# Performance work log

Measured on AMD Instinct MI355X. Metric: run time of the kernel, lower is better.

## Reference

```python
import jax, jax.numpy as jnp
import numpy as np

HIDDEN_DIM = 64


def setup_inputs() -> dict:
    key = jax.random.key(0)
    k1, k2, k3, k4, k5 = jax.random.split(key, 5)
    B, C, H, W = 4, HIDDEN_DIM, 80, 80
    query = jax.random.normal(k1, (B, C, H, W), dtype=jnp.float32)
    keys = jax.random.normal(k2, (B, C, H, W), dtype=jnp.float32)
    values = jax.random.normal(k3, (B, C, H, W), dtype=jnp.float32)
    # 1x1 conv == per-pixel linear: weight [C_out, C_in], bias [C_out]
    fan_in = C  # kernel_size=1 -> fan_in = C*1*1
    bound = 1.0 / np.sqrt(fan_in)
    Wq = jax.random.uniform(k4, (C, C), dtype=jnp.float32, minval=-bound, maxval=bound)
    bq = jax.random.uniform(k5, (C,), dtype=jnp.float32, minval=-bound, maxval=bound)
    return {"query": query, "keys": keys, "values": values, "Wq": Wq, "bq": bq}


def reference(query, keys, values, Wq, bq):
    B, C, H, W = query.shape
    scale = C ** (-0.5)
    # 1x1 conv projection of query
    qp = jnp.einsum('bchw,dc->bdhw', query, Wq) + bq[None, :, None, None]
    q = qp.reshape(B, C, H * W).transpose(0, 2, 1)       # [B, N, C]
    k = keys.reshape(B, C, H * W)                        # [B, C, N]
    attn = jax.nn.softmax(jnp.einsum('bnc,bcm->bnm', q, k) * scale, axis=-1)  # [B, N, N]
    v = values.reshape(B, C, H * W).transpose(0, 2, 1)   # [B, N, C]
    context = jnp.einsum('bnm,bmc->bnc', attn, v)        # [B, N, C]
    return context.transpose(0, 2, 1).reshape(B, C, H, W)
```

## Files before the change

kernel.cpp:

```cpp
#include <hip/hip_runtime.h>
#include <hip/hip_bf16.h>


#define NPIX 6400
#define SZ 1638400
#define SHIFT2 11.541560327111707f

typedef float f32x4 __attribute__((ext_vector_type(4)));
typedef short bf16x8 __attribute__((ext_vector_type(8)));

#if defined(__has_builtin)
#if __has_builtin(__builtin_amdgcn_sched_barrier)
#define SCHED_FENCE() __builtin_amdgcn_sched_barrier(0)
#endif
#if __has_builtin(__builtin_amdgcn_exp2f)
#define EXP2(x) __builtin_amdgcn_exp2f(x)
#endif
#endif
#ifndef SCHED_FENCE
#define SCHED_FENCE()
#endif
#ifndef EXP2
#define EXP2(x) exp2f(x)
#endif

__device__ __forceinline__ void split2(float x, short& h, short& l) {
  unsigned xb = __float_as_uint(x);
  h = (short)(xb >> 16);
  float r = x - __uint_as_float(xb & 0xffff0000u);
  l = (short)(__float_as_uint(r) >> 16);
}

__device__ __forceinline__ short rne_bf16(float x) {
  unsigned u = __float_as_uint(x);
  return (short)((u + 0x7fffu + ((u >> 16) & 1u)) >> 16);
}

__device__ __forceinline__ unsigned pk2(float a, float b) {
  __hip_bfloat162 t = __float22bfloat162_rn(make_float2(a, b));
  unsigned r;
  __builtin_memcpy(&r, &t, 4);
  return r;
}

__global__ __launch_bounds__(256, 4) void prep(
    const float* __restrict__ query, const float* __restrict__ keys,
    const float* __restrict__ values, const float* __restrict__ Wq,
    const float* __restrict__ bq, short* __restrict__ ws)
{
  const int tid = threadIdx.x;
  const int w = tid >> 6;
  const int lane = tid & 63, l16 = lane & 15, qq = lane >> 4;
  short* Qh = ws;          short* Ql = ws + SZ;
  short* Kh = ws + 2 * SZ; short* Kl = ws + 3 * SZ;
  short* Vh = ws + 4 * SZ;
  const int x = blockIdx.x;

  __shared__ float T[64 * 65];

  if (x < 400) {
    const int b = x / 100, t64 = x % 100;
    const int m0 = t64 * 64;
    const float* kb = keys + (size_t)b * 64 * NPIX;
    {
      const int ch = tid >> 2, ml = (tid & 3) * 4;
      const float* src = kb + (size_t)ch * NPIX + m0 + ml;
      #pragma unroll
      for (int u = 0; u < 4; ++u)
        *(float4*)&T[ch * 65 + ml + 16 * u] = *(const float4*)(src + 16 * u);
    }
    __syncthreads();
    const int mi = t64 * 4 + w;
    #pragma unroll
    for (int c0 = 0; c0 < 2; ++c0) {
      float t[8];
      #pragma unroll
      for (int j = 0; j < 8; ++j)
        t[j] = T[(32 * c0 + 8 * qq + j) * 65 + 16 * w + l16];
      bf16x8 h8, l8;
      #pragma unroll
      for (int j = 0; j < 8; ++j) { short h, l; split2(t[j], h, l); h8[j] = h; l8[j] = l; }
      const int off = ((b * 400 + mi) * 2 + c0) * 512 + lane * 8;
      *(bf16x8*)(Kh + off) = h8;
      *(bf16x8*)(Kl + off) = l8;
    }
  } else if (x < 800) {
    const int y = x - 400;
    const int b = y / 100, t64 = y % 100;
    const int r0 = t64 * 64;
    const float* qb = query + (size_t)b * 64 * NPIX;
    {
      const int ch = tid >> 2, ml = (tid & 3) * 4;
      const float* src = qb + (size_t)ch * NPIX + r0 + ml;
      #pragma unroll
      for (int u = 0; u < 4; ++u)
        *(float4*)&T[ch * 65 + ml + 16 * u] = *(const float4*)(src + 16 * u);
    }
    __syncthreads();

    {
      float xv[64];
      #pragma unroll
      for (int cin = 0; cin < 64; ++cin)
        xv[cin] = T[cin * 65 + lane];
      __syncthreads();

      #pragma unroll 4
      for (int c16 = 0; c16 < 16; ++c16) {
        const int co = __builtin_amdgcn_readfirstlane(16 * w + c16);
        const float* row = Wq + co * 64;
        float a = 0.f;
        #pragma unroll
        for (int cin = 0; cin < 64; ++cin)
          a += row[cin] * xv[cin];
        T[co * 65 + lane] = (a + bq[co]) * 0.18033688011112042f;
      }
    }
    __syncthreads();

    const int mi = t64 * 4 + w;
    #pragma unroll
    for (int c0 = 0; c0 < 2; ++c0) {
      float t[8];
      #pragma unroll
      for (int j = 0; j < 8; ++j)
        t[j] = T[(32 * c0 + 8 * qq + j) * 65 + 16 * w + l16];
      bf16x8 h8, l8;
      #pragma unroll
      for (int j = 0; j < 8; ++j) { short h, l; split2(t[j], h, l); h8[j] = h; l8[j] = l; }
      const int off = ((b * 400 + mi) * 2 + c0) * 512 + lane * 8;
      *(bf16x8*)(Qh + off) = h8;
      *(bf16x8*)(Ql + off) = l8;
    }
  } else {
    const int gw = (x - 800) * 4 + w;
    const int b = gw / 200, rest = gw % 200;
    const int i = rest / 2, half = rest % 2;
    const float* vb = values + (size_t)b * 64 * NPIX;
    #pragma unroll
    for (int cc = 0; cc < 2; ++cc) {
      const int ct = 2 * half + cc;
      #pragma unroll
      for (int mh = 0; mh < 2; ++mh) {
        const float* vp = vb + (size_t)(16 * ct + l16) * NPIX + 64 * i + 32 * mh + 8 * qq;
        const float4 a  = *(const float4*)vp;
        const float4 b4 = *(const float4*)(vp + 4);
        const float t[8] = {a.x, a.y, a.z, a.w, b4.x, b4.y, b4.z, b4.w};
        bf16x8 h8;
        #pragma unroll
        for (int j = 0; j < 8; ++j) h8[j] = rne_bf16(t[j]);
        const int off = (((b * 100 + i) * 8) + ct * 2 + mh) * 512 + lane * 8;
        *(bf16x8*)(Vh + off) = h8;
      }
    }
  }
}

__global__ __launch_bounds__(512, 1) void attn_main(
    const short* __restrict__ ws, float* __restrict__ out)
{
  const int tid  = threadIdx.x;
  const int w    = tid >> 6;
  const int lane = tid & 63;
  const int l16  = lane & 15, qq = lane >> 4;
  const int x = blockIdx.x;
  const int b      = x & 3;
  const int rowjob = x >> 2;
  const int rb     = rowjob * 64;

  const short* Qh = ws;
  const short* Kh = ws + 2 * SZ;
  const short* Vh = ws + 4 * SZ;
  float* ob = out + (size_t)b * 64 * NPIX;

  __shared__ char smem[43008];
  short* P   = ((short*)smem) + (w << 11);
  short* QL  = ((short*)smem) + 16384;
  float* OC  = (float*)smem;
  float* LST = (float*)(smem + 40960);

  bf16x8 qfh[4][2];
  {
    const short* qp = Qh + (size_t)((b * 400 + rowjob * 4) * 2) * 512 + lane * 8;
    #pragma unroll
    for (int s = 0; s < 4; ++s)
      #pragma unroll
      for (int c0 = 0; c0 < 2; ++c0) {
        qfh[s][c0] = *(const bf16x8*)(qp + (s * 2 + c0) * 512);
        *(bf16x8*)(QL + ((s * 2 + c0) * 64 + lane) * 8) =
            *(const bf16x8*)(qp + SZ + (s * 2 + c0) * 512);
      }
  }
  __syncthreads();

  f32x4 zero4 = {0.f, 0.f, 0.f, 0.f};
  f32x4 oacc[4][4];
  f32x4 lacc[4];
  #pragma unroll
  for (int ct = 0; ct < 4; ++ct)
    #pragma unroll
    for (int s = 0; s < 4; ++s) oacc[ct][s] = zero4;
  #pragma unroll
  for (int s = 0; s < 4; ++s) lacc[s] = zero4;

  bf16x8 onesA;
  #pragma unroll
  for (int j = 0; j < 8; ++j) onesA[j] = (short)0x3F80;

  bf16x8 kfh[2][2], kfl[2][2];
  bf16x8 vfh[4];

  auto loadK = [&](int i2) {
    const short* kp = Kh + (size_t)((b * 400 + 2 * i2) * 2) * 512 + lane * 8;
    #pragma unroll
    for (int mt = 0; mt < 2; ++mt)
      #pragma unroll
      for (int c0 = 0; c0 < 2; ++c0) {
        kfh[mt][c0] = *(const bf16x8*)(kp + (mt * 2 + c0) * 512);
        kfl[mt][c0] = *(const bf16x8*)(kp + SZ + (mt * 2 + c0) * 512);
      }
  };
  auto loadV = [&](int i2) {
    const short* vp = Vh + (size_t)((b * 100 + (i2 >> 1)) * 8) * 512 + lane * 8;
    #pragma unroll
    for (int ct = 0; ct < 4; ++ct)
      vfh[ct] = *(const bf16x8*)(vp + (ct * 2 + (i2 & 1)) * 512);
  };

  const int i0 = w * 25;
  loadK(i0);
  loadV(i0);

  for (int it = 0; it < 25; ++it) {
    const int i2 = i0 + it;
    const int inext = (it == 24) ? i0 : i2 + 1;

    f32x4 a0[4], a1[4];
    #pragma unroll
    for (int s = 0; s < 4; ++s) {
      f32x4 t0 = zero4, t1 = zero4;
      #pragma unroll
      for (int c0 = 0; c0 < 2; ++c0) {
        const bf16x8 ql = *(const bf16x8*)(QL + ((s * 2 + c0) * 64 + lane) * 8);
        t0 = __builtin_amdgcn_mfma_f32_16x16x32_bf16(kfh[0][c0], qfh[s][c0], t0, 0, 0, 0);
        t0 = __builtin_amdgcn_mfma_f32_16x16x32_bf16(kfh[0][c0], ql,         t0, 0, 0, 0);
        t0 = __builtin_amdgcn_mfma_f32_16x16x32_bf16(kfl[0][c0], qfh[s][c0], t0, 0, 0, 0);
        t1 = __builtin_amdgcn_mfma_f32_16x16x32_bf16(kfh[1][c0], qfh[s][c0], t1, 0, 0, 0);
        t1 = __builtin_amdgcn_mfma_f32_16x16x32_bf16(kfh[1][c0], ql,         t1, 0, 0, 0);
        t1 = __builtin_amdgcn_mfma_f32_16x16x32_bf16(kfl[1][c0], qfh[s][c0], t1, 0, 0, 0);
      }
      a0[s] = t0; a1[s] = t1;
    }

    SCHED_FENCE();
    loadK(inext);
    SCHED_FENCE();

    #pragma unroll
    for (int s = 0; s < 4; ++s) {
      float p0 = EXP2(a0[s][0] - SHIFT2), p1 = EXP2(a0[s][1] - SHIFT2);
      float p2 = EXP2(a0[s][2] - SHIFT2), p3 = EXP2(a0[s][3] - SHIFT2);
      float p4 = EXP2(a1[s][0] - SHIFT2), p5 = EXP2(a1[s][1] - SHIFT2);
      float p6 = EXP2(a1[s][2] - SHIFT2), p7 = EXP2(a1[s][3] - SHIFT2);
      union { unsigned u[2]; short4 s4; } ua, ub;
      ua.u[0] = pk2(p0, p1); ua.u[1] = pk2(p2, p3);
      ub.u[0] = pk2(p4, p5); ub.u[1] = pk2(p6, p7);
      const int gbase = (s * 4 + (qq >> 1)) * 16 + l16;
      *(short4*)(P + (gbase * 8 + 4 * (qq & 1))) = ua.s4;
      *(short4*)(P + ((gbase + 32) * 8 + 4 * (qq & 1))) = ub.s4;
    }

    bf16x8 pf[4];
    #pragma unroll
    for (int s = 0; s < 4; ++s)
      pf[s] = *(const bf16x8*)(P + (((s * 4 + qq) * 16 + l16) * 8));

    #pragma unroll
    for (int ct = 0; ct < 4; ++ct)
      #pragma unroll
      for (int s = 0; s < 4; ++s)
        oacc[ct][s] = __builtin_amdgcn_mfma_f32_16x16x32_bf16(vfh[ct], pf[s], oacc[ct][s], 0, 0, 0);
    #pragma unroll
    for (int s = 0; s < 4; ++s)
      lacc[s] = __builtin_amdgcn_mfma_f32_16x16x32_bf16(onesA, pf[s], lacc[s], 0, 0, 0);

    SCHED_FENCE();
    loadV(inext);
    SCHED_FENCE();
  }

  if (qq == 0) {
    #pragma unroll
    for (int s = 0; s < 4; ++s) LST[w * 64 + s * 16 + l16] = lacc[s][0];
  }
  __syncthreads();

  #pragma unroll
  for (int wp = 0; wp < 8; ++wp) {
    if (w == wp) {
      #pragma unroll
      for (int ct = 0; ct < 4; ++ct)
        #pragma unroll
        for (int s = 0; s < 4; ++s)
          #pragma unroll
          for (int r = 0; r < 4; ++r) {
            const int c = 16 * ct + 4 * qq + r;
            const int idx = c * 65 + 16 * s + l16;
            if (wp == 0) OC[idx] = oacc[ct][s][r];
            else         OC[idx] += oacc[ct][s][r];
          }
    }
    __syncthreads();
  }

  {
    const int r  = tid & 63;
    const int cg = tid >> 6;
    float lsum = 0.f;
    #pragma unroll
    for (int w2 = 0; w2 < 8; ++w2)
      lsum += LST[w2 * 64 + (r >> 4) * 16 + (r & 15)];
    const float inv = 1.0f / lsum;
    #pragma unroll
    for (int u = 0; u < 8; ++u) {
      const int c = cg * 8 + u;
      ob[(size_t)c * NPIX + rb + r] = OC[c * 65 + r] * inv;
    }
  }
}

extern "C" void kernel_launch(void* const* d_in, const int* in_sizes, int n_in,
                              void* d_out, int out_size, void* d_ws, size_t ws_size,
                              hipStream_t stream) {
  const float* query  = (const float*)d_in[0];
  const float* keys   = (const float*)d_in[1];
  const float* values = (const float*)d_in[2];
  const float* Wq     = (const float*)d_in[3];
  const float* bq     = (const float*)d_in[4];
  short* ws = (short*)d_ws;
  prep<<<dim3(1000), dim3(256), 0, stream>>>(query, keys, values, Wq, bq, ws);
  attn_main<<<dim3(400), dim3(512), 0, stream>>>(ws, (float*)d_out);
}
```

Measured before the change: 177.0 us.

## Split attention work across waves by row/column tiles with shared K staging

```diff
diff --git a/kernel.cpp b/kernel.cpp
--- a/kernel.cpp
+++ b/kernel.cpp
@@ -10,15 +10,9 @@
 typedef short bf16x8 __attribute__((ext_vector_type(8)));
 
 #if defined(__has_builtin)
-#if __has_builtin(__builtin_amdgcn_sched_barrier)
-#define SCHED_FENCE() __builtin_amdgcn_sched_barrier(0)
-#endif
 #if __has_builtin(__builtin_amdgcn_exp2f)
 #define EXP2(x) __builtin_amdgcn_exp2f(x)
 #endif
-#endif
-#ifndef SCHED_FENCE
-#define SCHED_FENCE()
 #endif
 #ifndef EXP2
 #define EXP2(x) exp2f(x)
@@ -41,6 +35,11 @@
   unsigned r;
   __builtin_memcpy(&r, &t, 4);
   return r;
+}
+
+__device__ __forceinline__ float bf2f(short s) {
+  unsigned u = ((unsigned)(unsigned short)s) << 16;
+  return __uint_as_float(u);
 }
 
 __global__ __launch_bounds__(256, 4) void prep(
@@ -156,13 +155,17 @@
   }
 }
 
-__global__ __launch_bounds__(512, 1) void attn_main(
+__global__ __launch_bounds__(512, 2) void attn_main(
     const short* __restrict__ ws, float* __restrict__ out)
 {
   const int tid  = threadIdx.x;
   const int w    = tid >> 6;
   const int lane = tid & 63;
   const int l16  = lane & 15, qq = lane >> 4;
+  const int hp   = w >> 2;
+  const int rs   = w & 3;
+  const int cp   = w >> 2;
+  const int rv   = w & 3;
   const int x = blockIdx.x;
   const int b      = x & 3;
   const int rowjob = x >> 2;
@@ -173,154 +176,128 @@
   const short* Vh = ws + 4 * SZ;
   float* ob = out + (size_t)b * 64 * NPIX;
 
-  __shared__ char smem[43008];
-  short* P   = ((short*)smem) + (w << 11);
-  short* QL  = ((short*)smem) + 16384;
+  __shared__ char smem[25088];
+  short* KST = (short*)smem;
+  short* Ps  = ((short*)smem) + 8192;
+  float* LST = (float*)(smem + 24576);
   float* OC  = (float*)smem;
-  float* LST = (float*)(smem + 40960);
-
-  bf16x8 qfh[4][2];
+
+  bf16x8 qh[2], ql[2];
   {
-    const short* qp = Qh + (size_t)((b * 400 + rowjob * 4) * 2) * 512 + lane * 8;
-    #pragma unroll
-    for (int s = 0; s < 4; ++s)
-      #pragma unroll
-      for (int c0 = 0; c0 < 2; ++c0) {
-        qfh[s][c0] = *(const bf16x8*)(qp + (s * 2 + c0) * 512);
-        *(bf16x8*)(QL + ((s * 2 + c0) * 64 + lane) * 8) =
-            *(const bf16x8*)(qp + SZ + (s * 2 + c0) * 512);
-      }
+    const short* qp = Qh + (size_t)((b * 400 + rowjob * 4 + rs) * 2) * 512 + lane * 8;
+    #pragma unroll
+    for (int c0 = 0; c0 < 2; ++c0) {
+      qh[c0] = *(const bf16x8*)(qp + c0 * 512);
+      ql[c0] = *(const bf16x8*)(qp + SZ + c0 * 512);
+    }
+  }
+
+  f32x4 zero4 = {0.f, 0.f, 0.f, 0.f};
+  f32x4 oacc[2];
+  oacc[0] = zero4; oacc[1] = zero4;
+  float lsum = 0.f;
+
+  {
+    const short* gk = Kh + (size_t)(b * 400) * 1024;
+    bf16x8 s0 = *(const bf16x8*)(gk + w * 512 + lane * 8);
+    bf16x8 s1 = *(const bf16x8*)(gk + SZ + w * 512 + lane * 8);
+    *(bf16x8*)(KST + w * 512 + lane * 8) = s0;
+    *(bf16x8*)(KST + 4096 + w * 512 + lane * 8) = s1;
   }
   __syncthreads();
 
-  f32x4 zero4 = {0.f, 0.f, 0.f, 0.f};
-  f32x4 oacc[4][4];
-  f32x4 lacc[4];
-  #pragma unroll
-  for (int ct = 0; ct < 4; ++ct)
-    #pragma unroll
-    for (int s = 0; s < 4; ++s) oacc[ct][s] = zero4;
-  #pragma unroll
-  for (int s = 0; s < 4; ++s) lacc[s] = zero4;
-
-  bf16x8 onesA;
-  #pragma unroll
-  for (int j = 0; j < 8; ++j) onesA[j] = (short)0x3F80;
-
-  bf16x8 kfh[2][2], kfl[2][2];
-  bf16x8 vfh[4];
-
-  auto loadK = [&](int i2) {
-    const short* kp = Kh + (size_t)((b * 400 + 2 * i2) * 2) * 512 + lane * 8;
-    #pragma unroll
-    for (int mt = 0; mt < 2; ++mt)
-      #pragma unroll
-      for (int c0 = 0; c0 < 2; ++c0) {
-        kfh[mt][c0] = *(const bf16x8*)(kp + (mt * 2 + c0) * 512);
-        kfl[mt][c0] = *(const bf16x8*)(kp + SZ + (mt * 2 + c0) * 512);
-      }
-  };
-  auto loadV = [&](int i2) {
-    const short* vp = Vh + (size_t)((b * 100 + (i2 >> 1)) * 8) * 512 + lane * 8;
-    #pragma unroll
-    for (int ct = 0; ct < 4; ++ct)
-      vfh[ct] = *(const bf16x8*)(vp + (ct * 2 + (i2 & 1)) * 512);
-  };
-
-  const int i0 = w * 25;
-  loadK(i0);
-  loadV(i0);
-
-  for (int it = 0; it < 25; ++it) {
-    const int i2 = i0 + it;
-    const int inext = (it == 24) ? i0 : i2 + 1;
-
-    f32x4 a0[4], a1[4];
-    #pragma unroll
-    for (int s = 0; s < 4; ++s) {
-      f32x4 t0 = zero4, t1 = zero4;
-      #pragma unroll
-      for (int c0 = 0; c0 < 2; ++c0) {
-        const bf16x8 ql = *(const bf16x8*)(QL + ((s * 2 + c0) * 64 + lane) * 8);
-        t0 = __builtin_amdgcn_mfma_f32_16x16x32_bf16(kfh[0][c0], qfh[s][c0], t0, 0, 0, 0);
-        t0 = __builtin_amdgcn_mfma_f32_16x16x32_bf16(kfh[0][c0], ql,         t0, 0, 0, 0);
-        t0 = __builtin_amdgcn_mfma_f32_16x16x32_bf16(kfl[0][c0], qfh[s][c0], t0, 0, 0, 0);
-        t1 = __builtin_amdgcn_mfma_f32_16x16x32_bf16(kfh[1][c0], qfh[s][c0], t1, 0, 0, 0);
-        t1 = __builtin_amdgcn_mfma_f32_16x16x32_bf16(kfh[1][c0], ql,         t1, 0, 0, 0);
-        t1 = __builtin_amdgcn_mfma_f32_16x16x32_bf16(kfl[1][c0], qfh[s][c0], t1, 0, 0, 0);
-      }
-      a0[s] = t0; a1[s] = t1;
-    }
-
-    SCHED_FENCE();
-    loadK(inext);
-    SCHED_FENCE();
-
-    #pragma unroll
-    for (int s = 0; s < 4; ++s) {
-      float p0 = EXP2(a0[s][0] - SHIFT2), p1 = EXP2(a0[s][1] - SHIFT2);
-      float p2 = EXP2(a0[s][2] - SHIFT2), p3 = EXP2(a0[s][3] - SHIFT2);
-      float p4 = EXP2(a1[s][0] - SHIFT2), p5 = EXP2(a1[s][1] - SHIFT2);
-      float p6 = EXP2(a1[s][2] - SHIFT2), p7 = EXP2(a1[s][3] - SHIFT2);
+  for (int i = 0; i < 100; ++i) {
+    bf16x8 vfh[2][2];
+    {
+      const short* vp = Vh + (size_t)((b * 100 + i) * 8) * 512 + lane * 8;
+      #pragma unroll
+      for (int cti = 0; cti < 2; ++cti)
+        #pragma unroll
+        for (int mh = 0; mh < 2; ++mh)
+          vfh[cti][mh] = *(const bf16x8*)(vp + ((2 * cp + cti) * 2 + mh) * 512);
+    }
+
+    f32x4 a0 = zero4, a1 = zero4;
+    #pragma unroll
+    for (int c0 = 0; c0 < 2; ++c0) {
+      const bf16x8 kh0 = *(const bf16x8*)(KST + ((2 * hp + 0) * 2 + c0) * 512 + lane * 8);
+      const bf16x8 kl0 = *(const bf16x8*)(KST + 4096 + ((2 * hp + 0) * 2 + c0) * 512 + lane * 8);
+      const bf16x8 kh1 = *(const bf16x8*)(KST + ((2 * hp + 1) * 2 + c0) * 512 + lane * 8);
+      const bf16x8 kl1 = *(const bf16x8*)(KST + 4096 + ((2 * hp + 1) * 2 + c0) * 512 + lane * 8);
+      a0 = __builtin_amdgcn_mfma_f32_16x16x32_bf16(kh0, qh[c0], a0, 0, 0, 0);
+      a0 = __builtin_amdgcn_mfma_f32_16x16x32_bf16(kh0, ql[c0], a0, 0, 0, 0);
+      a0 = __builtin_amdgcn_mfma_f32_16x16x32_bf16(kl0, qh[c0], a0, 0, 0, 0);
+      a1 = __builtin_amdgcn_mfma_f32_16x16x32_bf16(kh1, qh[c0], a1, 0, 0, 0);
+      a1 = __builtin_amdgcn_mfma_f32_16x16x32_bf16(kh1, ql[c0], a1, 0, 0, 0);
+      a1 = __builtin_amdgcn_mfma_f32_16x16x32_bf16(kl1, qh[c0], a1, 0, 0, 0);
+    }
+
+    {
+      short* PW = Ps + hp * 2048;
+      float p0 = EXP2(a0[0] - SHIFT2), p1 = EXP2(a0[1] - SHIFT2);
+      float p2 = EXP2(a0[2] - SHIFT2), p3 = EXP2(a0[3] - SHIFT2);
+      float p4 = EXP2(a1[0] - SHIFT2), p5 = EXP2(a1[1] - SHIFT2);
+      float p6 = EXP2(a1[2] - SHIFT2), p7 = EXP2(a1[3] - SHIFT2);
       union { unsigned u[2]; short4 s4; } ua, ub;
       ua.u[0] = pk2(p0, p1); ua.u[1] = pk2(p2, p3);
       ub.u[0] = pk2(p4, p5); ub.u[1] = pk2(p6, p7);
-      const int gbase = (s * 4 + (qq >> 1)) * 16 + l16;
-      *(short4*)(P + (gbase * 8 + 4 * (qq & 1))) = ua.s4;
-      *(short4*)(P + ((gbase + 32) * 8 + 4 * (qq & 1))) = ub.s4;
-    }
-
-    bf16x8 pf[4];
-    #pragma unroll
-    for (int s = 0; s < 4; ++s)
-      pf[s] = *(const bf16x8*)(P + (((s * 4 + qq) * 16 + l16) * 8));
-
-    #pragma unroll
-    for (int ct = 0; ct < 4; ++ct)
-      #pragma unroll
-      for (int s = 0; s < 4; ++s)
-        oacc[ct][s] = __builtin_amdgcn_mfma_f32_16x16x32_bf16(vfh[ct], pf[s], oacc[ct][s], 0, 0, 0);
-    #pragma unroll
-    for (int s = 0; s < 4; ++s)
-      lacc[s] = __builtin_amdgcn_mfma_f32_16x16x32_bf16(onesA, pf[s], lacc[s], 0, 0, 0);
-
-    SCHED_FENCE();
-    loadV(inext);
-    SCHED_FENCE();
-  }
-
-  if (qq == 0) {
-    #pragma unroll
-    for (int s = 0; s < 4; ++s) LST[w * 64 + s * 16 + l16] = lacc[s][0];
+      const int gbase = (rs * 4 + (qq >> 1)) * 16 + l16;
+      *(short4*)(PW + (gbase * 8 + 4 * (qq & 1))) = ua.s4;
+      *(short4*)(PW + ((gbase + 32) * 8 + 4 * (qq & 1))) = ub.s4;
+    }
+    __syncthreads();
+
+    bf16x8 s0, s1;
+    {
+      const int inext = (i == 99) ? i : i + 1;
+      const short* gk = Kh + (size_t)(b * 400 + 4 * inext) * 1024;
+      s0 = *(const bf16x8*)(gk + w * 512 + lane * 8);
+      s1 = *(const bf16x8*)(gk + SZ + w * 512 + lane * 8);
+    }
+
+    {
+      const bf16x8 pf0 = *(const bf16x8*)(Ps + ((rv * 4 + qq) * 16 + l16) * 8);
+      const bf16x8 pf1 = *(const bf16x8*)(Ps + 2048 + ((rv * 4 + qq) * 16 + l16) * 8);
+      #pragma unroll
+      for (int cti = 0; cti < 2; ++cti) {
+        oacc[cti] = __builtin_amdgcn_mfma_f32_16x16x32_bf16(vfh[cti][0], pf0, oacc[cti], 0, 0, 0);
+        oacc[cti] = __builtin_amdgcn_mfma_f32_16x16x32_bf16(vfh[cti][1], pf1, oacc[cti], 0, 0, 0);
+      }
+      if (cp == 0) {
+        float t = 0.f;
+        #pragma unroll
+        for (int j = 0; j < 8; ++j) t += bf2f(pf0[j]);
+        #pragma unroll
+        for (int j = 0; j < 8; ++j) t += bf2f(pf1[j]);
+        lsum += t;
+      }
+    }
+
+    *(bf16x8*)(KST + w * 512 + lane * 8) = s0;
+    *(bf16x8*)(KST + 4096 + w * 512 + lane * 8) = s1;
+    __syncthreads();
+  }
+
+  if (cp == 0) {
+    lsum += __shfl_xor(lsum, 16);
+    lsum += __shfl_xor(lsum, 32);
+    if (qq == 0) LST[rv * 16 + l16] = lsum;
   }
   __syncthreads();
 
   #pragma unroll
-  for (int wp = 0; wp < 8; ++wp) {
-    if (w == wp) {
-      #pragma unroll
-      for (int ct = 0; ct < 4; ++ct)
-        #pragma unroll
-        for (int s = 0; s < 4; ++s)
-          #pragma unroll
-          for (int r = 0; r < 4; ++r) {
-            const int c = 16 * ct + 4 * qq + r;
-            const int idx = c * 65 + 16 * s + l16;
-            if (wp == 0) OC[idx] = oacc[ct][s][r];
-            else         OC[idx] += oacc[ct][s][r];
-          }
-    }
-    __syncthreads();
-  }
+  for (int cti = 0; cti < 2; ++cti)
+    #pragma unroll
+    for (int r = 0; r < 4; ++r) {
+      const int c = 16 * (2 * cp + cti) + 4 * qq + r;
+      OC[c * 65 + 16 * rv + l16] = oacc[cti][r];
+    }
+  __syncthreads();
 
   {
     const int r  = tid & 63;
     const int cg = tid >> 6;
-    float lsum = 0.f;
-    #pragma unroll
-    for (int w2 = 0; w2 < 8; ++w2)
-      lsum += LST[w2 * 64 + (r >> 4) * 16 + (r & 15)];
-    const float inv = 1.0f / lsum;
+    const float inv = 1.0f / LST[(r >> 4) * 16 + (r & 15)];
     #pragma unroll
     for (int u = 0; u < 8; ++u) {
       const int c = cg * 8 + u;
```

Result: slower. 190.1 us (+7.4%).
